# Kernel tuning notes

Hardware: AMD Instinct MI355X
Metric: run time of the kernel (lower is better)

The kernel has to match this reference:

```python
import jax, jax.numpy as jnp
import numpy as np

VOCAB = 1024   # must equal HID (embedding Linear consumes vocab-sized x)
HID = 1024
EMB = 256
NOS = 12
B, M = 512, 8
TEMP = 1.0


def setup_inputs() -> dict:
    key = jax.random.key(0)
    ks = jax.random.split(key, 12)
    N = B * M
    target = jax.random.normal(ks[0], (B, M, HID), jnp.float32)
    # precomputed standard Gumbel noise per step (training=True path)
    u = jax.random.uniform(ks[1], (NOS, N, VOCAB), jnp.float32, 1e-6, 1.0 - 1e-6)
    gumbels = -jnp.log(-jnp.log(u))
    sh = 1.0 / np.sqrt(HID)
    sv = 1.0 / np.sqrt(VOCAB)
    sos = 0.01 * jax.random.normal(ks[2], (EMB,), jnp.float32)
    W_ih = jax.random.uniform(ks[3], (HID, EMB), jnp.float32, -sh, sh)
    b_ih = jax.random.uniform(ks[4], (HID,), jnp.float32, -sh, sh)
    W_hh = jax.random.uniform(ks[5], (HID, HID), jnp.float32, -sh, sh)
    b_hh = jax.random.uniform(ks[6], (HID,), jnp.float32, -sh, sh)
    W_out = jax.random.uniform(ks[7], (VOCAB, HID), jnp.float32, -sh, sh)
    b_out = jax.random.uniform(ks[8], (VOCAB,), jnp.float32, -sh, sh)
    W_emb = jax.random.uniform(ks[9], (EMB, VOCAB), jnp.float32, -sv, sv)
    b_emb = jax.random.uniform(ks[10], (EMB,), jnp.float32, -sv, sv)
    return dict(target=target, gumbels=gumbels, sos=sos,
                W_ih=W_ih, b_ih=b_ih, W_hh=W_hh, b_hh=b_hh,
                W_out=W_out, b_out=b_out, W_emb=W_emb, b_emb=b_emb)


def reference(target, gumbels, sos, W_ih, b_ih, W_hh, b_hh, W_out, b_out, W_emb, b_emb):
    b_, m_, h_ = target.shape
    prev = target.reshape(b_ * m_, h_)            # [N, HID]
    e0 = jnp.broadcast_to(sos, (prev.shape[0], sos.shape[0]))  # [N, EMB]

    def step(carry, g):
        prev_h, e = carry
        h = jnp.tanh(e @ W_ih.T + b_ih + prev_h @ W_hh.T + b_hh)   # RNNCell
        logits = h @ W_out.T + b_out                               # [N, VOCAB]
        x = jax.nn.softmax((logits + g) / TEMP, axis=-1)           # gumbel-softmax
        e_next = x @ W_emb.T + b_emb                               # [N, EMB]
        return (h, e_next), x

    _, xs = jax.lax.scan(step, (prev, e0), gumbels)  # xs: [NOS, N, VOCAB]
    return jnp.transpose(xs, (1, 0, 2))              # [N, NOS, VOCAB]
```

## Files before the change

kernel.cpp:

```cpp
#include <hip/hip_runtime.h>

#define N_TOT 4096
#define HIDN  1024
#define EMBD  256
#define VOC   1024
#define NSTEP 12

typedef __bf16 bf16;
typedef _Float16 h16;
typedef __bf16 bf16x8 __attribute__((ext_vector_type(8)));
typedef __bf16 bf16x4 __attribute__((ext_vector_type(4)));
typedef _Float16 h16x8 __attribute__((ext_vector_type(8)));
typedef float  f32x4  __attribute__((ext_vector_type(4)));

static __device__ __forceinline__ f32x4 mfma16(bf16x8 a, bf16x8 b, f32x4 c) {
  return __builtin_amdgcn_mfma_f32_16x16x32_bf16(a, b, c, 0, 0, 0);
}

static __device__ __forceinline__ void gload16(const bf16* g, bf16* l) {
  __builtin_amdgcn_global_load_lds(
      (const __attribute__((address_space(1))) void*)g,
      (__attribute__((address_space(3))) void*)l, 16, 0, 0);
}


__global__ void prep_kernel(const float* __restrict__ Wih, const float* __restrict__ Whh,
                            const float* __restrict__ Wout, const float* __restrict__ Wemb,
                            const float* __restrict__ target, const float* __restrict__ sos,
                            const float* __restrict__ bih, const float* __restrict__ bhh,
                            bf16* __restrict__ wih_b, bf16* __restrict__ whh_b,
                            bf16* __restrict__ wout_b, bf16* __restrict__ wemb_b,
                            bf16* __restrict__ hbuf, bf16* __restrict__ ebuf,
                            float* __restrict__ bias1) {
  for (int q = blockIdx.x * blockDim.x + threadIdx.x; q < 1966336;
       q += blockDim.x * gridDim.x) {
    if (q < 1703936) {
      const float* s; bf16* d; int o;
      if (q < 65536)        { s = Wih;    d = wih_b;  o = q; }
      else if (q < 327680)  { s = Whh;    d = whh_b;  o = q - 65536; }
      else if (q < 589824)  { s = Wout;   d = wout_b; o = q - 327680; }
      else if (q < 655360)  { s = Wemb;   d = wemb_b; o = q - 589824; }
      else                  { s = target; d = hbuf;   o = q - 655360; }
      f32x4 v = *(const f32x4*)&s[(size_t)o * 4];
      bf16x4 b; b[0] = (bf16)v.x; b[1] = (bf16)v.y; b[2] = (bf16)v.z; b[3] = (bf16)v.w;
      *(bf16x4*)&d[(size_t)o * 4] = b;
    } else if (q < 1966080) {
      int o = q - 1703936;
      f32x4 v = *(const f32x4*)&sos[(o & 63) * 4];
      bf16x4 b; b[0] = (bf16)v.x; b[1] = (bf16)v.y; b[2] = (bf16)v.z; b[3] = (bf16)v.w;
      *(bf16x4*)&ebuf[(size_t)o * 4] = b;
    } else {
      int o = q - 1966080;
      f32x4 a = *(const f32x4*)&bih[o * 4];
      f32x4 c = *(const f32x4*)&bhh[o * 4];
      f32x4 r; r.x = a.x + c.x; r.y = a.y + c.y; r.z = a.z + c.z; r.w = a.w + c.w;
      *(f32x4*)&bias1[o * 4] = r;
    }
  }
}


__global__ __launch_bounds__(256)
void rnn_cell_kernel(const bf16* __restrict__ e,
                     const bf16* __restrict__ hprev,
                     const bf16* __restrict__ Wih,
                     const bf16* __restrict__ Whh,
                     const float* __restrict__ bias,
                     bf16* __restrict__ hnew)
{
  __shared__ bf16 As[2 * 128 * 64];
  __shared__ bf16 Bs[2 * 64 * 64];
  const int tid = threadIdx.x;
  const int lane = tid & 63;
  const int w = tid >> 6;
  const int wr = w >> 1, wc = w & 1;
  const int id = (blockIdx.x & 7) * (gridDim.x >> 3) + (blockIdx.x >> 3);
  const int m0 = (id >> 4) * 128;
  const int n0 = (id & 15) * 64;
  const int lr = lane & 15, lk = lane >> 4;
  const int srow = lane >> 3;
  const int scol = (((lane & 7) ^ srow) << 3);

  auto stage = [&](int t, int bsel) {
    const bf16 *A, *B; int K, k0;
    if (t < 4) { A = e;     B = Wih; K = EMBD; k0 = t << 6; }
    else       { A = hprev; B = Whh; K = HIDN; k0 = (t - 4) << 6; }
    bf16* Ad = As + bsel * 8192 + w * 512;
    bf16* Bd = Bs + bsel * 4096 + w * 512;
#pragma unroll
    for (int r = 0; r < 4; ++r)
      gload16(&A[(size_t)(m0 + r * 32 + w * 8 + srow) * K + k0 + scol], Ad + r * 2048);
#pragma unroll
    for (int r = 0; r < 2; ++r)
      gload16(&B[(size_t)(n0 + r * 32 + w * 8 + srow) * K + k0 + scol], Bd + r * 2048);
  };

  f32x4 acc[4][2] = {};
  stage(0, 0);
  __syncthreads();
  for (int t = 0; t < 20; ++t) {
    if (t < 19) stage(t + 1, (t + 1) & 1);
    const bf16* Ab = As + (t & 1) * 8192;
    const bf16* Bb = Bs + (t & 1) * 4096;
#pragma unroll
    for (int kk = 0; kk < 2; ++kk) {
      bf16x8 af[4], bfr[2];
#pragma unroll
      for (int mi = 0; mi < 4; ++mi) {
        int row = wr * 64 + mi * 16 + lr;
        af[mi] = *(const bf16x8*)&Ab[row * 64 + ((((kk << 2) | lk) ^ (row & 7)) << 3)];
      }
#pragma unroll
      for (int ni = 0; ni < 2; ++ni) {
        int row = wc * 32 + ni * 16 + lr;
        bfr[ni] = *(const bf16x8*)&Bb[row * 64 + ((((kk << 2) | lk) ^ (row & 7)) << 3)];
      }
#pragma unroll
      for (int mi = 0; mi < 4; ++mi)
#pragma unroll
        for (int ni = 0; ni < 2; ++ni)
          acc[mi][ni] = mfma16(af[mi], bfr[ni], acc[mi][ni]);
    }
    __syncthreads();
  }

#pragma unroll
  for (int mi = 0; mi < 4; ++mi) {
    int rowb = m0 + wr * 64 + mi * 16 + lk * 4;
#pragma unroll
    for (int ni = 0; ni < 2; ++ni) {
      int col = n0 + wc * 32 + ni * 16 + lr;
      float bs = bias[col];
#pragma unroll
      for (int j = 0; j < 4; ++j) {
        float v = tanhf(acc[mi][ni][j] + bs);
        hnew[(size_t)(rowb + j) * HIDN + col] = (bf16)v;
      }
    }
  }
}


__global__ __launch_bounds__(256)
void logits_kernel(const bf16* __restrict__ h,
                   const bf16* __restrict__ Wout,
                   const float* __restrict__ bout,
                   h16* __restrict__ lbuf)
{
  __shared__ bf16 As[2 * 128 * 64];
  __shared__ bf16 Bs[2 * 64 * 64];
  const int tid = threadIdx.x;
  const int lane = tid & 63;
  const int w = tid >> 6;
  const int wr = w >> 1, wc = w & 1;
  const int id = (blockIdx.x & 7) * (gridDim.x >> 3) + (blockIdx.x >> 3);
  const int m0 = (id >> 4) * 128;
  const int n0 = (id & 15) * 64;
  const int lr = lane & 15, lk = lane >> 4;
  const int srow = lane >> 3;
  const int scol = (((lane & 7) ^ srow) << 3);

  auto stage = [&](int t, int bsel) {
    int k0 = t << 6;
    bf16* Ad = As + bsel * 8192 + w * 512;
    bf16* Bd = Bs + bsel * 4096 + w * 512;
#pragma unroll
    for (int r = 0; r < 4; ++r)
      gload16(&h[(size_t)(m0 + r * 32 + w * 8 + srow) * HIDN + k0 + scol], Ad + r * 2048);
#pragma unroll
    for (int r = 0; r < 2; ++r)
      gload16(&Wout[(size_t)(n0 + r * 32 + w * 8 + srow) * HIDN + k0 + scol], Bd + r * 2048);
  };

  f32x4 acc[4][2] = {};
  stage(0, 0);
  __syncthreads();
  for (int t = 0; t < 16; ++t) {
    if (t < 15) stage(t + 1, (t + 1) & 1);
    const bf16* Ab = As + (t & 1) * 8192;
    const bf16* Bb = Bs + (t & 1) * 4096;
#pragma unroll
    for (int kk = 0; kk < 2; ++kk) {
      bf16x8 af[4], bfr[2];
#pragma unroll
      for (int mi = 0; mi < 4; ++mi) {
        int row = wr * 64 + mi * 16 + lr;
        af[mi] = *(const bf16x8*)&Ab[row * 64 + ((((kk << 2) | lk) ^ (row & 7)) << 3)];
      }
#pragma unroll
      for (int ni = 0; ni < 2; ++ni) {
        int row = wc * 32 + ni * 16 + lr;
        bfr[ni] = *(const bf16x8*)&Bb[row * 64 + ((((kk << 2) | lk) ^ (row & 7)) << 3)];
      }
#pragma unroll
      for (int mi = 0; mi < 4; ++mi)
#pragma unroll
        for (int ni = 0; ni < 2; ++ni)
          acc[mi][ni] = mfma16(af[mi], bfr[ni], acc[mi][ni]);
    }
    __syncthreads();
  }

#pragma unroll
  for (int mi = 0; mi < 4; ++mi) {
    int rowb = m0 + wr * 64 + mi * 16 + lk * 4;
#pragma unroll
    for (int ni = 0; ni < 2; ++ni) {
      int col = n0 + wc * 32 + ni * 16 + lr;
      float bs = bout[col];
#pragma unroll
      for (int j = 0; j < 4; ++j) {
        int row = rowb + j;
        lbuf[(size_t)row * VOC + col] = (h16)(acc[mi][ni][j] + bs);
      }
    }
  }
}


__global__ __launch_bounds__(512)
void softmax_emb_kernel(const h16* __restrict__ lbuf,
                        const float* __restrict__ gum,
                        const bf16* __restrict__ Wemb,
                        const float* __restrict__ bemb,
                        float* __restrict__ out,
                        bf16* __restrict__ enext,
                        int step)
{
  __shared__ bf16 xs[16 * 1032];
  const int tid = threadIdx.x;
  const int lane = tid & 63;
  const int w = tid >> 6;
  const int n0 = blockIdx.x * 16;

  for (int rr = 0; rr < 2; ++rr) {
    int r = w + rr * 8;
    const h16* lrow = lbuf + (size_t)(n0 + r) * VOC;
    const float* grow = gum + (size_t)(n0 + r) * VOC;
    float s[16];
    float m = -1e30f;
#pragma unroll
    for (int i = 0; i < 2; ++i) {
      h16x8 lv = *(const h16x8*)&lrow[i * 512 + lane * 8];
      f32x4 g0 = *(const f32x4*)&grow[i * 512 + lane * 8];
      f32x4 g1 = *(const f32x4*)&grow[i * 512 + lane * 8 + 4];
#pragma unroll
      for (int j = 0; j < 4; ++j) {
        float f0 = (float)lv[j] + g0[j];
        float f1 = (float)lv[4 + j] + g1[j];
        s[i * 8 + j] = f0; s[i * 8 + 4 + j] = f1;
        m = fmaxf(m, fmaxf(f0, f1));
      }
    }
#pragma unroll
    for (int off = 32; off; off >>= 1) m = fmaxf(m, __shfl_xor(m, off));
    float sum = 0.f;
#pragma unroll
    for (int i = 0; i < 16; ++i) { s[i] = __expf(s[i] - m); sum += s[i]; }
#pragma unroll
    for (int off = 32; off; off >>= 1) sum += __shfl_xor(sum, off);
    float inv = 1.0f / sum;
    float* orow = out + ((size_t)(n0 + r) * NSTEP + step) * VOC;
#pragma unroll
    for (int i = 0; i < 2; ++i) {
      f32x4 v0, v1;
      bf16x8 bv;
#pragma unroll
      for (int j = 0; j < 4; ++j) {
        float x0 = s[i * 8 + j] * inv;
        float x1 = s[i * 8 + 4 + j] * inv;
        v0[j] = x0; v1[j] = x1;
        bv[j] = (bf16)x0; bv[4 + j] = (bf16)x1;
      }
      *(f32x4*)&orow[i * 512 + lane * 8] = v0;
      *(f32x4*)&orow[i * 512 + lane * 8 + 4] = v1;
      *(bf16x8*)&xs[r * 1032 + i * 512 + lane * 8] = bv;
    }
  }
  __syncthreads();

  const int lr = lane & 15, lk = lane >> 4;
  f32x4 acc[2] = {};
  for (int k0 = 0; k0 < VOC; k0 += 32) {
    bf16x8 a = *(bf16x8*)&xs[lr * 1032 + k0 + lk * 8];
#pragma unroll
    for (int ni = 0; ni < 2; ++ni) {
      int col = w * 32 + ni * 16 + lr;
      bf16x8 b = *(const bf16x8*)&Wemb[(size_t)col * VOC + k0 + lk * 8];
      acc[ni] = mfma16(a, b, acc[ni]);
    }
  }
#pragma unroll
  for (int ni = 0; ni < 2; ++ni) {
    int col = w * 32 + ni * 16 + lr;
    float bb = bemb[col];
#pragma unroll
    for (int j = 0; j < 4; ++j) {
      int n = n0 + lk * 4 + j;
      enext[(size_t)n * EMBD + col] = (bf16)(acc[ni][j] + bb);
    }
  }
}


extern "C" void kernel_launch(void* const* d_in, const int* in_sizes, int n_in,
                              void* d_out, int out_size, void* d_ws, size_t ws_size,
                              hipStream_t stream) {
  const float* target  = (const float*)d_in[0];
  const float* gumbels = (const float*)d_in[1];
  const float* sos     = (const float*)d_in[2];
  const float* W_ih    = (const float*)d_in[3];
  const float* b_ih    = (const float*)d_in[4];
  const float* W_hh    = (const float*)d_in[5];
  const float* b_hh    = (const float*)d_in[6];
  const float* W_out   = (const float*)d_in[7];
  const float* b_out   = (const float*)d_in[8];
  const float* W_emb   = (const float*)d_in[9];
  const float* b_emb   = (const float*)d_in[10];
  float* out = (float*)d_out;

  char* ws = (char*)d_ws;
  bf16* wih_b  = (bf16*)(ws);
  bf16* whh_b  = (bf16*)(ws + (1u << 20));
  bf16* wout_b = (bf16*)(ws + (3u << 20));
  bf16* wemb_b = (bf16*)(ws + (5u << 20));
  float* bias1 = (float*)(ws + (6u << 20));
  bf16* hbuf0  = (bf16*)(ws + (7u << 20));
  bf16* hbuf1  = (bf16*)(ws + (15u << 20));
  bf16* ebuf   = (bf16*)(ws + (23u << 20));
  h16*  lbuf   = (h16*) (ws + (25u << 20));

  prep_kernel<<<2048, 256, 0, stream>>>(W_ih, W_hh, W_out, W_emb, target, sos,
                                        b_ih, b_hh, wih_b, whh_b, wout_b, wemb_b,
                                        hbuf0, ebuf, bias1);

  bf16* hb[2] = {hbuf0, hbuf1};
  for (int t = 0; t < NSTEP; ++t) {
    bf16* hp = hb[t & 1];
    bf16* hn = hb[(t + 1) & 1];
    rnn_cell_kernel<<<(N_TOT / 128) * (HIDN / 64), 256, 0, stream>>>(
        ebuf, hp, wih_b, whh_b, bias1, hn);
    logits_kernel<<<(N_TOT / 128) * (VOC / 64), 256, 0, stream>>>(
        hn, wout_b, b_out, lbuf);
    softmax_emb_kernel<<<N_TOT / 16, 512, 0, stream>>>(
        lbuf, gumbels + (size_t)t * N_TOT * VOC, wemb_b, b_emb, out, ebuf, t);
  }
}
```

Baseline: 753.1 us.

## Enlarge GEMM tiles to 128x128 with 8 waves and 4-stage async LDS pipeline

```diff
diff --git a/kernel.cpp b/kernel.cpp
--- a/kernel.cpp
+++ b/kernel.cpp
@@ -12,6 +12,9 @@
 typedef __bf16 bf16x4 __attribute__((ext_vector_type(4)));
 typedef _Float16 h16x8 __attribute__((ext_vector_type(8)));
 typedef float  f32x4  __attribute__((ext_vector_type(4)));
+
+#define VMCNT(n) asm volatile("s_waitcnt vmcnt(" #n ")" ::: "memory")
+#define MEMFENCE() asm volatile("" ::: "memory")
 
 static __device__ __forceinline__ f32x4 mfma16(bf16x8 a, bf16x8 b, f32x4 c) {
   return __builtin_amdgcn_mfma_f32_16x16x32_bf16(a, b, c, 0, 0, 0);
@@ -60,7 +63,7 @@
 }
 
 
-__global__ __launch_bounds__(256)
+__global__ __launch_bounds__(512)
 void rnn_cell_kernel(const bf16* __restrict__ e,
                      const bf16* __restrict__ hprev,
                      const bf16* __restrict__ Wih,
@@ -68,15 +71,14 @@
                      const float* __restrict__ bias,
                      bf16* __restrict__ hnew)
 {
-  __shared__ bf16 As[2 * 128 * 64];
-  __shared__ bf16 Bs[2 * 64 * 64];
+  __shared__ bf16 lds[4 * 16384];
   const int tid = threadIdx.x;
   const int lane = tid & 63;
   const int w = tid >> 6;
-  const int wr = w >> 1, wc = w & 1;
+  const int wr = w >> 2, wc = w & 3;
   const int id = (blockIdx.x & 7) * (gridDim.x >> 3) + (blockIdx.x >> 3);
-  const int m0 = (id >> 4) * 128;
-  const int n0 = (id & 15) * 64;
+  const int m0 = (id >> 3) * 128;
+  const int n0 = (id & 7) * 128;
   const int lr = lane & 15, lk = lane >> 4;
   const int srow = lane >> 3;
   const int scol = (((lane & 7) ^ srow) << 3);
@@ -85,23 +87,31 @@
     const bf16 *A, *B; int K, k0;
     if (t < 4) { A = e;     B = Wih; K = EMBD; k0 = t << 6; }
     else       { A = hprev; B = Whh; K = HIDN; k0 = (t - 4) << 6; }
-    bf16* Ad = As + bsel * 8192 + w * 512;
-    bf16* Bd = Bs + bsel * 4096 + w * 512;
-#pragma unroll
-    for (int r = 0; r < 4; ++r)
-      gload16(&A[(size_t)(m0 + r * 32 + w * 8 + srow) * K + k0 + scol], Ad + r * 2048);
+    bf16* base = lds + bsel * 16384;
 #pragma unroll
     for (int r = 0; r < 2; ++r)
-      gload16(&B[(size_t)(n0 + r * 32 + w * 8 + srow) * K + k0 + scol], Bd + r * 2048);
+      gload16(&A[(size_t)(m0 + w * 16 + r * 8 + srow) * K + k0 + scol],
+              base + (w * 16 + r * 8) * 64);
+#pragma unroll
+    for (int r = 0; r < 2; ++r)
+      gload16(&B[(size_t)(n0 + w * 16 + r * 8 + srow) * K + k0 + scol],
+              base + 8192 + (w * 16 + r * 8) * 64);
   };
 
+  const int NT = 20;
   f32x4 acc[4][2] = {};
-  stage(0, 0);
-  __syncthreads();
-  for (int t = 0; t < 20; ++t) {
-    if (t < 19) stage(t + 1, (t + 1) & 1);
-    const bf16* Ab = As + (t & 1) * 8192;
-    const bf16* Bb = Bs + (t & 1) * 4096;
+  stage(0, 0); stage(1, 1); stage(2, 2);
+  VMCNT(8);
+  for (int t = 0; t < NT; ++t) {
+    MEMFENCE();
+    __builtin_amdgcn_s_barrier();
+    MEMFENCE();
+    if (t + 3 < NT) stage(t + 3, (t + 3) & 3);
+    if (t <= NT - 4)      VMCNT(8);
+    else if (t == NT - 3) VMCNT(4);
+    else if (t == NT - 2) VMCNT(0);
+    const bf16* Ab = lds + (t & 3) * 16384;
+    const bf16* Bb = Ab + 8192;
 #pragma unroll
     for (int kk = 0; kk < 2; ++kk) {
       bf16x8 af[4], bfr[2];
@@ -121,7 +131,6 @@
         for (int ni = 0; ni < 2; ++ni)
           acc[mi][ni] = mfma16(af[mi], bfr[ni], acc[mi][ni]);
     }
-    __syncthreads();
   }
 
 #pragma unroll
@@ -132,53 +141,58 @@
       int col = n0 + wc * 32 + ni * 16 + lr;
       float bs = bias[col];
 #pragma unroll
-      for (int j = 0; j < 4; ++j) {
-        float v = tanhf(acc[mi][ni][j] + bs);
-        hnew[(size_t)(rowb + j) * HIDN + col] = (bf16)v;
-      }
-    }
-  }
-}
-
-
-__global__ __launch_bounds__(256)
+      for (int j = 0; j < 4; ++j)
+        hnew[(size_t)(rowb + j) * HIDN + col] = (bf16)tanhf(acc[mi][ni][j] + bs);
+    }
+  }
+}
+
+
+__global__ __launch_bounds__(512)
 void logits_kernel(const bf16* __restrict__ h,
                    const bf16* __restrict__ Wout,
                    const float* __restrict__ bout,
                    h16* __restrict__ lbuf)
 {
-  __shared__ bf16 As[2 * 128 * 64];
-  __shared__ bf16 Bs[2 * 64 * 64];
+  __shared__ bf16 lds[4 * 16384];
   const int tid = threadIdx.x;
   const int lane = tid & 63;
   const int w = tid >> 6;
-  const int wr = w >> 1, wc = w & 1;
+  const int wr = w >> 2, wc = w & 3;
   const int id = (blockIdx.x & 7) * (gridDim.x >> 3) + (blockIdx.x >> 3);
-  const int m0 = (id >> 4) * 128;
-  const int n0 = (id & 15) * 64;
+  const int m0 = (id >> 3) * 128;
+  const int n0 = (id & 7) * 128;
   const int lr = lane & 15, lk = lane >> 4;
   const int srow = lane >> 3;
   const int scol = (((lane & 7) ^ srow) << 3);
 
   auto stage = [&](int t, int bsel) {
     int k0 = t << 6;
-    bf16* Ad = As + bsel * 8192 + w * 512;
-    bf16* Bd = Bs + bsel * 4096 + w * 512;
-#pragma unroll
-    for (int r = 0; r < 4; ++r)
-      gload16(&h[(size_t)(m0 + r * 32 + w * 8 + srow) * HIDN + k0 + scol], Ad + r * 2048);
+    bf16* base = lds + bsel * 16384;
 #pragma unroll
     for (int r = 0; r < 2; ++r)
-      gload16(&Wout[(size_t)(n0 + r * 32 + w * 8 + srow) * HIDN + k0 + scol], Bd + r * 2048);
+      gload16(&h[(size_t)(m0 + w * 16 + r * 8 + srow) * HIDN + k0 + scol],
+              base + (w * 16 + r * 8) * 64);
+#pragma unroll
+    for (int r = 0; r < 2; ++r)
+      gload16(&Wout[(size_t)(n0 + w * 16 + r * 8 + srow) * HIDN + k0 + scol],
+              base + 8192 + (w * 16 + r * 8) * 64);
   };
 
+  const int NT = 16;
   f32x4 acc[4][2] = {};
-  stage(0, 0);
-  __syncthreads();
-  for (int t = 0; t < 16; ++t) {
-    if (t < 15) stage(t + 1, (t + 1) & 1);
-    const bf16* Ab = As + (t & 1) * 8192;
-    const bf16* Bb = Bs + (t & 1) * 4096;
+  stage(0, 0); stage(1, 1); stage(2, 2);
+  VMCNT(8);
+  for (int t = 0; t < NT; ++t) {
+    MEMFENCE();
+    __builtin_amdgcn_s_barrier();
+    MEMFENCE();
+    if (t + 3 < NT) stage(t + 3, (t + 3) & 3);
+    if (t <= NT - 4)      VMCNT(8);
+    else if (t == NT - 3) VMCNT(4);
+    else if (t == NT - 2) VMCNT(0);
+    const bf16* Ab = lds + (t & 3) * 16384;
+    const bf16* Bb = Ab + 8192;
 #pragma unroll
     for (int kk = 0; kk < 2; ++kk) {
       bf16x8 af[4], bfr[2];
@@ -198,7 +212,6 @@
         for (int ni = 0; ni < 2; ++ni)
           acc[mi][ni] = mfma16(af[mi], bfr[ni], acc[mi][ni]);
     }
-    __syncthreads();
   }
 
 #pragma unroll
@@ -338,9 +351,9 @@
   for (int t = 0; t < NSTEP; ++t) {
     bf16* hp = hb[t & 1];
     bf16* hn = hb[(t + 1) & 1];
-    rnn_cell_kernel<<<(N_TOT / 128) * (HIDN / 64), 256, 0, stream>>>(
+    rnn_cell_kernel<<<(N_TOT / 128) * (HIDN / 128), 512, 0, stream>>>(
         ebuf, hp, wih_b, whh_b, bias1, hn);
-    logits_kernel<<<(N_TOT / 128) * (VOC / 64), 256, 0, stream>>>(
+    logits_kernel<<<(N_TOT / 128) * (VOC / 128), 512, 0, stream>>>(
         hn, wout_b, b_out, lbuf);
     softmax_emb_kernel<<<N_TOT / 16, 512, 0, stream>>>(
         lbuf, gumbels + (size_t)t * N_TOT * VOC, wemb_b, b_emb, out, ebuf, t);
```

Measured after the change: 647.8 us. -14.0%, faster.

## Triple-buffer GEMM K-loop with explicit vmcnt waits and a single barrier

Applied to the files above, without the earlier changes.

```diff
diff --git a/kernel.cpp b/kernel.cpp
--- a/kernel.cpp
+++ b/kernel.cpp
@@ -12,6 +12,9 @@
 typedef __bf16 bf16x4 __attribute__((ext_vector_type(4)));
 typedef _Float16 h16x8 __attribute__((ext_vector_type(8)));
 typedef float  f32x4  __attribute__((ext_vector_type(4)));
+
+#define VMCNT(n) asm volatile("s_waitcnt vmcnt(" #n ")" ::: "memory")
+#define MEMFENCE() asm volatile("" ::: "memory")
 
 static __device__ __forceinline__ f32x4 mfma16(bf16x8 a, bf16x8 b, f32x4 c) {
   return __builtin_amdgcn_mfma_f32_16x16x32_bf16(a, b, c, 0, 0, 0);
@@ -60,7 +63,72 @@
 }
 
 
-__global__ __launch_bounds__(256)
+template <bool TWO, int NT>
+static __device__ __forceinline__ void pipe_gemm(
+    const bf16* __restrict__ A0, const bf16* __restrict__ B0, int K0,
+    const bf16* __restrict__ A1, const bf16* __restrict__ B1, int K1,
+    bf16* lds, int m0, int n0, int w, int lane, f32x4 acc[4][2])
+{
+  const int wr = w >> 1, wc = w & 1;
+  const int lr = lane & 15, lk = lane >> 4;
+  const int srow = lane >> 3;
+  const int scol = (((lane & 7) ^ srow) << 3);
+
+  auto stage = [&](int t, int bsel) {
+    const bf16 *A, *B; int K, k0;
+    if (TWO && t < 4) { A = A0; B = B0; K = K0; k0 = t << 6; }
+    else if (TWO)     { A = A1; B = B1; K = K1; k0 = (t - 4) << 6; }
+    else              { A = A0; B = B0; K = K0; k0 = t << 6; }
+    bf16* base = lds + bsel * 12288;
+#pragma unroll
+    for (int r = 0; r < 4; ++r)
+      gload16(&A[(size_t)(m0 + w * 32 + r * 8 + srow) * K + k0 + scol],
+              base + (w * 32 + r * 8) * 64);
+#pragma unroll
+    for (int r = 0; r < 2; ++r)
+      gload16(&B[(size_t)(n0 + w * 16 + r * 8 + srow) * K + k0 + scol],
+              base + 8192 + (w * 16 + r * 8) * 64);
+  };
+
+  stage(0, 0); stage(1, 1);
+  VMCNT(6);
+  for (int t = 0; t < NT; ++t) {
+    MEMFENCE();
+    __builtin_amdgcn_s_barrier();
+    MEMFENCE();
+    if (t + 2 < NT) {
+      int b = (t + 2) % 3;
+      stage(t + 2, b);
+      VMCNT(6);
+    } else if (t == NT - 2) {
+      VMCNT(0);
+    }
+    const bf16* Ab = lds + (t % 3) * 12288;
+    const bf16* Bb = Ab + 8192;
+#pragma unroll
+    for (int kk = 0; kk < 2; ++kk) {
+      bf16x8 af[4], bfr[2];
+#pragma unroll
+      for (int mi = 0; mi < 4; ++mi) {
+        int row = wr * 64 + mi * 16 + lr;
+        af[mi] = *(const bf16x8*)&Ab[row * 64 + ((((kk << 2) | lk) ^ (row & 7)) << 3)];
+      }
+#pragma unroll
+      for (int ni = 0; ni < 2; ++ni) {
+        int row = wc * 32 + ni * 16 + lr;
+        bfr[ni] = *(const bf16x8*)&Bb[row * 64 + ((((kk << 2) | lk) ^ (row & 7)) << 3)];
+      }
+#pragma unroll
+      for (int mi = 0; mi < 4; ++mi)
+#pragma unroll
+        for (int ni = 0; ni < 2; ++ni)
+          acc[mi][ni] = mfma16(af[mi], bfr[ni], acc[mi][ni]);
+    }
+  }
+}
+
+
+__global__ __launch_bounds__(256, 2)
 void rnn_cell_kernel(const bf16* __restrict__ e,
                      const bf16* __restrict__ hprev,
                      const bf16* __restrict__ Wih,
@@ -68,61 +136,18 @@
                      const float* __restrict__ bias,
                      bf16* __restrict__ hnew)
 {
-  __shared__ bf16 As[2 * 128 * 64];
-  __shared__ bf16 Bs[2 * 64 * 64];
+  __shared__ bf16 lds[3 * 12288];
   const int tid = threadIdx.x;
   const int lane = tid & 63;
   const int w = tid >> 6;
   const int wr = w >> 1, wc = w & 1;
-  const int id = (blockIdx.x & 7) * (gridDim.x >> 3) + (blockIdx.x >> 3);
+  const int id = (blockIdx.x & 7) * 64 + (blockIdx.x >> 3);
   const int m0 = (id >> 4) * 128;
   const int n0 = (id & 15) * 64;
   const int lr = lane & 15, lk = lane >> 4;
-  const int srow = lane >> 3;
-  const int scol = (((lane & 7) ^ srow) << 3);
-
-  auto stage = [&](int t, int bsel) {
-    const bf16 *A, *B; int K, k0;
-    if (t < 4) { A = e;     B = Wih; K = EMBD; k0 = t << 6; }
-    else       { A = hprev; B = Whh; K = HIDN; k0 = (t - 4) << 6; }
-    bf16* Ad = As + bsel * 8192 + w * 512;
-    bf16* Bd = Bs + bsel * 4096 + w * 512;
-#pragma unroll
-    for (int r = 0; r < 4; ++r)
-      gload16(&A[(size_t)(m0 + r * 32 + w * 8 + srow) * K + k0 + scol], Ad + r * 2048);
-#pragma unroll
-    for (int r = 0; r < 2; ++r)
-      gload16(&B[(size_t)(n0 + r * 32 + w * 8 + srow) * K + k0 + scol], Bd + r * 2048);
-  };
 
   f32x4 acc[4][2] = {};
-  stage(0, 0);
-  __syncthreads();
-  for (int t = 0; t < 20; ++t) {
-    if (t < 19) stage(t + 1, (t + 1) & 1);
-    const bf16* Ab = As + (t & 1) * 8192;
-    const bf16* Bb = Bs + (t & 1) * 4096;
-#pragma unroll
-    for (int kk = 0; kk < 2; ++kk) {
-      bf16x8 af[4], bfr[2];
-#pragma unroll
-      for (int mi = 0; mi < 4; ++mi) {
-        int row = wr * 64 + mi * 16 + lr;
-        af[mi] = *(const bf16x8*)&Ab[row * 64 + ((((kk << 2) | lk) ^ (row & 7)) << 3)];
-      }
-#pragma unroll
-      for (int ni = 0; ni < 2; ++ni) {
-        int row = wc * 32 + ni * 16 + lr;
-        bfr[ni] = *(const bf16x8*)&Bb[row * 64 + ((((kk << 2) | lk) ^ (row & 7)) << 3)];
-      }
-#pragma unroll
-      for (int mi = 0; mi < 4; ++mi)
-#pragma unroll
-        for (int ni = 0; ni < 2; ++ni)
-          acc[mi][ni] = mfma16(af[mi], bfr[ni], acc[mi][ni]);
-    }
-    __syncthreads();
-  }
+  pipe_gemm<true, 20>(e, Wih, EMBD, hprev, Whh, HIDN, lds, m0, n0, w, lane, acc);
 
 #pragma unroll
   for (int mi = 0; mi < 4; ++mi) {
@@ -132,74 +157,31 @@
       int col = n0 + wc * 32 + ni * 16 + lr;
       float bs = bias[col];
 #pragma unroll
-      for (int j = 0; j < 4; ++j) {
-        float v = tanhf(acc[mi][ni][j] + bs);
-        hnew[(size_t)(rowb + j) * HIDN + col] = (bf16)v;
-      }
-    }
-  }
-}
-
-
-__global__ __launch_bounds__(256)
+      for (int j = 0; j < 4; ++j)
+        hnew[(size_t)(rowb + j) * HIDN + col] = (bf16)tanhf(acc[mi][ni][j] + bs);
+    }
+  }
+}
+
+
+__global__ __launch_bounds__(256, 2)
 void logits_kernel(const bf16* __restrict__ h,
                    const bf16* __restrict__ Wout,
                    const float* __restrict__ bout,
                    h16* __restrict__ lbuf)
 {
-  __shared__ bf16 As[2 * 128 * 64];
-  __shared__ bf16 Bs[2 * 64 * 64];
+  __shared__ bf16 lds[3 * 12288];
   const int tid = threadIdx.x;
   const int lane = tid & 63;
   const int w = tid >> 6;
   const int wr = w >> 1, wc = w & 1;
-  const int id = (blockIdx.x & 7) * (gridDim.x >> 3) + (blockIdx.x >> 3);
+  const int id = (blockIdx.x & 7) * 64 + (blockIdx.x >> 3);
   const int m0 = (id >> 4) * 128;
   const int n0 = (id & 15) * 64;
   const int lr = lane & 15, lk = lane >> 4;
-  const int srow = lane >> 3;
-  const int scol = (((lane & 7) ^ srow) << 3);
-
-  auto stage = [&](int t, int bsel) {
-    int k0 = t << 6;
-    bf16* Ad = As + bsel * 8192 + w * 512;
-    bf16* Bd = Bs + bsel * 4096 + w * 512;
-#pragma unroll
-    for (int r = 0; r < 4; ++r)
-      gload16(&h[(size_t)(m0 + r * 32 + w * 8 + srow) * HIDN + k0 + scol], Ad + r * 2048);
-#pragma unroll
-    for (int r = 0; r < 2; ++r)
-      gload16(&Wout[(size_t)(n0 + r * 32 + w * 8 + srow) * HIDN + k0 + scol], Bd + r * 2048);
-  };
 
   f32x4 acc[4][2] = {};
-  stage(0, 0);
-  __syncthreads();
-  for (int t = 0; t < 16; ++t) {
-    if (t < 15) stage(t + 1, (t + 1) & 1);
-    const bf16* Ab = As + (t & 1) * 8192;
-    const bf16* Bb = Bs + (t & 1) * 4096;
-#pragma unroll
-    for (int kk = 0; kk < 2; ++kk) {
-      bf16x8 af[4], bfr[2];
-#pragma unroll
-      for (int mi = 0; mi < 4; ++mi) {
-        int row = wr * 64 + mi * 16 + lr;
-        af[mi] = *(const bf16x8*)&Ab[row * 64 + ((((kk << 2) | lk) ^ (row & 7)) << 3)];
-      }
-#pragma unroll
-      for (int ni = 0; ni < 2; ++ni) {
-        int row = wc * 32 + ni * 16 + lr;
-        bfr[ni] = *(const bf16x8*)&Bb[row * 64 + ((((kk << 2) | lk) ^ (row & 7)) << 3)];
-      }
-#pragma unroll
-      for (int mi = 0; mi < 4; ++mi)
-#pragma unroll
-        for (int ni = 0; ni < 2; ++ni)
-          acc[mi][ni] = mfma16(af[mi], bfr[ni], acc[mi][ni]);
-    }
-    __syncthreads();
-  }
+  pipe_gemm<false, 16>(h, Wout, HIDN, nullptr, nullptr, 0, lds, m0, n0, w, lane, acc);
 
 #pragma unroll
   for (int mi = 0; mi < 4; ++mi) {
```

Result: faster. 655.1 us (-13.0%).
